# Kernel tuning notes

Measured on AMD Instinct MI355X. Metric: run time of the kernel, lower is better.

The kernel has to match this reference:

```python
import jax, jax.numpy as jnp
import numpy as np

N, V, E, C_IN, C_OUT = 4, 4096, 2048, 64, 64


def setup_inputs() -> dict:
    key = jax.random.key(0)
    k_x, k_h, k_th = jax.random.split(key, 3)
    x = jax.random.normal(k_x, (N, V, C_IN), dtype=jnp.float32)
    H = (jax.random.uniform(k_h, (N, V, E)) < 0.05).astype(jnp.float32)
    # guarantee every vertex and every hyperedge has degree >= 1 (code divides by degree)
    v_idx = jnp.arange(V)
    H = H.at[:, v_idx, v_idx % E].set(1.0)
    # xavier_uniform for theta
    limit = float(np.sqrt(6.0 / (C_IN + C_OUT)))
    theta = jax.random.uniform(k_th, (C_IN, C_OUT), minval=-limit, maxval=limit, dtype=jnp.float32)
    bias = jnp.zeros((C_OUT,), dtype=jnp.float32)
    return {"x": x, "H": H, "theta": theta, "bias": bias}


def reference(x, H, theta, bias):
    # x: [N,V,C], H: [N,V,E] incidence, theta: [C,O], bias: [O]
    # Original builds diag_embed(1/deg) and multiplies; equivalent to direct
    # per-row / per-column scaling of H (same math, no NxVxV / NxExE diagonals).
    dv = 1.0 / H.sum(-1)            # [N,V] vertex degrees
    de = 1.0 / H.sum(1)             # [N,E] hyperedge degrees
    y = jnp.einsum('nvc,co->nvo', x, theta)          # [N,V,O]
    HDe = H * de[:, None, :]                          # H @ De  -> [N,V,E]
    y = jnp.einsum('nvc,nve->nec', y, HDe)            # vertex -> edge  [N,E,O]
    HDv = H * dv[:, :, None]                          # Dv @ H -> [N,V,E]
    y = jnp.einsum('nec,nve->nvc', y, HDv)            # edge -> vertex  [N,V,O]
    return y + bias[None, None, :]
```

## Files before the change

kernel.cpp:

```cpp
#include <hip/hip_runtime.h>
#include <hip/hip_bf16.h>
#include <stdint.h>

#define N_B 4
#define NV 4096
#define NE 2048

typedef float    f32x4  __attribute__((ext_vector_type(4)));
typedef __bf16   bf16x8 __attribute__((ext_vector_type(8)));
typedef unsigned short u16;
typedef u16      u16x8  __attribute__((ext_vector_type(8)));
typedef uint32_t u32x4  __attribute__((ext_vector_type(4)));

__device__ __forceinline__ u16 f2bf_rne(float f) {
    uint32_t u = __builtin_bit_cast(uint32_t, f);
    u += 0x7FFFu + ((u >> 16) & 1u);
    return (u16)(u >> 16);
}
__device__ __forceinline__ float bf2f(u16 h) {
    uint32_t u = ((uint32_t)h) << 16;
    return __builtin_bit_cast(float, u);
}
__device__ __forceinline__ f32x4 mfma_bf16(u16x8 a, u16x8 b, f32x4 c) {
    return __builtin_amdgcn_mfma_f32_16x16x32_bf16(
        __builtin_bit_cast(bf16x8, a), __builtin_bit_cast(bf16x8, b), c, 0, 0, 0);
}
__device__ __forceinline__ u16x8 expand8(uint32_t byte) {
    u32x4 w;
#pragma unroll
    for (int p = 0; p < 4; ++p) {
        const uint32_t lo = (byte >> (2 * p)) & 1u;
        const uint32_t hi = (byte >> (2 * p + 1)) & 1u;
        w[p] = (lo | (hi << 16)) * 0x3F80u;
    }
    return __builtin_bit_cast(u16x8, w);
}

__global__ __launch_bounds__(256) void k_prep(const float* __restrict__ H,
                                              const float* __restrict__ x,
                                              const float* __restrict__ th,
                                              uint32_t* __restrict__ HB,
                                              uint32_t* __restrict__ HT,
                                              u16* __restrict__ Yh,
                                              u16* __restrict__ Yl) {
    __shared__ float smem[64 * 65];
    const int bid = blockIdx.x;
    const int t = threadIdx.x;

    if (bid < 8192) {
        float (*tile)[65] = (float(*)[65])smem;
        const int ex = bid & 31, vy = (bid >> 5) & 63, n = bid >> 11;
        const int e0 = ex * 64, v0 = vy * 64;
        const float* __restrict__ Hn = H + ((size_t)n * NV + v0) * NE + e0;

#pragma unroll
        for (int i = 0; i < 4; ++i) {
            const int idx = i * 256 + t;
            const int row = idx >> 4;
            const int q = (idx & 15) * 4;
            const float4 hv = *(const float4*)(Hn + (size_t)row * NE + q);
            tile[row][q] = hv.x; tile[row][q + 1] = hv.y;
            tile[row][q + 2] = hv.z; tile[row][q + 3] = hv.w;
        }
        __syncthreads();

        if (t < 128) {
            const int v = t >> 1, we = t & 1;
            uint32_t u = 0;
#pragma unroll
            for (int j = 0; j < 32; ++j)
                u |= (tile[v][we * 32 + j] != 0.0f) ? (1u << j) : 0u;
            HB[(((size_t)n * (NV / 16) + ((v0 + v) >> 4)) * (NE / 32) + (e0 >> 5) + we) * 16 +
               ((v0 + v) & 15)] = u;
        } else {
            const int e = (t - 128) >> 1, wv = t & 1;
            uint32_t u = 0;
#pragma unroll
            for (int j = 0; j < 32; ++j)
                u |= (tile[wv * 32 + j][e] != 0.0f) ? (1u << j) : 0u;
            HT[(((size_t)n * (NE / 16) + ((e0 + e) >> 4)) * (NV / 32) + (v0 >> 5) + wv) * 16 +
               ((e0 + e) & 15)] = u;
        }
    } else {
        float (*ts)[65] = (float(*)[65])smem;
        const int bx = bid - 8192;
        const int n = bx >> 6, v0 = (bx & 63) * 64;

#pragma unroll
        for (int i = 0; i < 4; ++i) {
            const int idx = i * 256 + t;
            const int row = idx >> 4, q = (idx & 15) * 4;
            const float4 tv = *(const float4*)&th[(size_t)row * 64 + q];
            ts[row][q] = tv.x; ts[row][q + 1] = tv.y;
            ts[row][q + 2] = tv.z; ts[row][q + 3] = tv.w;
        }
        __syncthreads();

        const int v4 = (t & 15) * 4;
        const int c4 = (t >> 4) * 4;
        const float* __restrict__ xb = x + ((size_t)(n * NV + v0 + v4)) * 64;

        float acc[4][4] = {};
#pragma unroll
        for (int kb = 0; kb < 16; ++kb) {
            float4 xr[4];
#pragma unroll
            for (int j = 0; j < 4; ++j)
                xr[j] = *(const float4*)(xb + (size_t)j * 64 + kb * 4);
#pragma unroll
            for (int kk = 0; kk < 4; ++kk) {
                const int k = kb * 4 + kk;
                float tv[4], xv[4];
#pragma unroll
                for (int i = 0; i < 4; ++i) tv[i] = ts[k][c4 + i];
                xv[0] = xr[0][kk]; xv[1] = xr[1][kk];
                xv[2] = xr[2][kk]; xv[3] = xr[3][kk];
#pragma unroll
                for (int i = 0; i < 4; ++i)
#pragma unroll
                    for (int j = 0; j < 4; ++j) acc[i][j] += tv[i] * xv[j];
            }
        }
#pragma unroll
        for (int i = 0; i < 4; ++i) {
            ushort4 hi, lo;
            u16 h;
            h = f2bf_rne(acc[i][0]); hi.x = h; lo.x = f2bf_rne(acc[i][0] - bf2f(h));
            h = f2bf_rne(acc[i][1]); hi.y = h; lo.y = f2bf_rne(acc[i][1] - bf2f(h));
            h = f2bf_rne(acc[i][2]); hi.z = h; lo.z = f2bf_rne(acc[i][2] - bf2f(h));
            h = f2bf_rne(acc[i][3]); hi.w = h; lo.w = f2bf_rne(acc[i][3] - bf2f(h));
            const size_t o = ((size_t)n * 64 + c4 + i) * NV + v0 + v4;
            *(ushort4*)&Yh[o] = hi;
            *(ushort4*)&Yl[o] = lo;
        }
    }
}

__global__ __launch_bounds__(256, 8) void k_v2e(const uint32_t* __restrict__ HT,
                                                const uint32_t* __restrict__ HB,
                                                const u16* __restrict__ Yh,
                                                const u16* __restrict__ Yl,
                                                float* __restrict__ P2,
                                                float* __restrict__ de,
                                                float* __restrict__ dv) {
    const int t = threadIdx.x;
    const int s2 = gridDim.y;
    const int lin = blockIdx.x + 32 * (blockIdx.y + s2 * blockIdx.z);
    const int nb = 32 * s2 * N_B;

    if (t < 64) {
        const int total = N_B * NE + N_B * NV;
        for (int id = lin * 64 + t; id < total; id += nb * 64) {
            if (id < N_B * NE) {
                const int n_ = id >> 11, e = id & (NE - 1);
                const uint32_t* p =
                    HT + ((size_t)n_ * (NE / 16) + (e >> 4)) * ((NV / 32) * 16) + (e & 15);
                uint32_t s = 0;
#pragma unroll 4
                for (int wv = 0; wv < NV / 32; ++wv) s += __popc(p[(size_t)wv * 16]);
                de[id] = (float)s;
            } else {
                const int j = id - N_B * NE;
                const int n_ = j >> 12, v = j & (NV - 1);
                const uint32_t* p =
                    HB + ((size_t)n_ * (NV / 16) + (v >> 4)) * ((NE / 32) * 16) + (v & 15);
                uint32_t s = 0;
#pragma unroll 4
                for (int we = 0; we < NE / 32; ++we) s += __popc(p[(size_t)we * 16]);
                dv[j] = (float)s;
            }
        }
    }

    const int wid = (lin & 7) * (nb >> 3) + (lin >> 3);
    const int n   = wid / (32 * s2);
    const int rem = wid % (32 * s2);
    const int sp  = rem >> 5;
    const int e0  = (rem & 31) * 64;

    const int krange = NV / s2;
    const int kk0 = sp * krange;
    const int S   = krange / 32;

    const int w = t >> 6, l = t & 63;
    const int lq = l >> 4, lr = l & 15;
    const int sh = lq * 8;
    const int hstride = (NV / 32) * 16;

    const uint32_t* __restrict__ ht =
        HT + ((size_t)n * (NE / 16) + (e0 >> 4)) * hstride + (kk0 >> 5) * 16 + lr;
    const u16* __restrict__ ybh = Yh + ((size_t)n * 64 + w * 16 + lr) * NV + kk0 + lq * 8;
    const u16* __restrict__ ybl = Yl + ((size_t)n * 64 + w * 16 + lr) * NV + kk0 + lq * 8;

    f32x4 acc0 = {0.f,0.f,0.f,0.f}, acc1 = acc0, acc2 = acc0, acc3 = acc0;

    uint32_t A[2][4];
#pragma unroll
    for (int d = 0; d < 2; ++d) {
        A[d][0] = ht[0 * hstride + d * 16];
        A[d][1] = ht[1 * hstride + d * 16];
        A[d][2] = ht[2 * hstride + d * 16];
        A[d][3] = ht[3 * hstride + d * 16];
    }
    u16x8 BH[2], BL[2];
    BH[0] = *(const u16x8*)ybh;
    BL[0] = *(const u16x8*)ybl;

#define V2E_STEP(s, u, GA, GB)                                                \
    {                                                                         \
        const uint32_t a0 = A[u][0], a1 = A[u][1], a2 = A[u][2], a3 = A[u][3];\
        if (GA) {                                                             \
            A[u][0] = ht[0 * hstride + ((s) + 2) * 16];                       \
            A[u][1] = ht[1 * hstride + ((s) + 2) * 16];                       \
            A[u][2] = ht[2 * hstride + ((s) + 2) * 16];                       \
            A[u][3] = ht[3 * hstride + ((s) + 2) * 16];                       \
        }                                                                     \
        if (GB) {                                                             \
            BH[((u) + 1) & 1] = *(const u16x8*)(ybh + ((s) + 1) * 32);        \
            BL[((u) + 1) & 1] = *(const u16x8*)(ybl + ((s) + 1) * 32);        \
        }                                                                     \
        const u16x8 bh = BH[u], bl = BL[u];                                   \
        u16x8 a;                                                              \
        a = expand8((a0 >> sh) & 0xFF);                                       \
        acc0 = mfma_bf16(a, bh, acc0); acc0 = mfma_bf16(a, bl, acc0);         \
        a = expand8((a1 >> sh) & 0xFF);                                       \
        acc1 = mfma_bf16(a, bh, acc1); acc1 = mfma_bf16(a, bl, acc1);         \
        a = expand8((a2 >> sh) & 0xFF);                                       \
        acc2 = mfma_bf16(a, bh, acc2); acc2 = mfma_bf16(a, bl, acc2);         \
        a = expand8((a3 >> sh) & 0xFF);                                       \
        acc3 = mfma_bf16(a, bh, acc3); acc3 = mfma_bf16(a, bl, acc3);         \
    }

    int sb = 0;
    for (; sb < S - 2; sb += 2) {
        V2E_STEP(sb + 0, 0, true, true)
        V2E_STEP(sb + 1, 1, true, true)
    }
    V2E_STEP(sb + 0, 0, false, true)
    V2E_STEP(sb + 1, 1, false, false)
#undef V2E_STEP

    float* pb = P2 + (((size_t)sp * N_B + n) * 64 + w * 16 + lr) * NE + e0 + lq * 4;
    *(f32x4*)(pb + 0)  = acc0;
    *(f32x4*)(pb + 16) = acc1;
    *(f32x4*)(pb + 32) = acc2;
    *(f32x4*)(pb + 48) = acc3;
}

__global__ __launch_bounds__(256) void k_red2(const float* __restrict__ P2,
                                              const float* __restrict__ de,
                                              u16* __restrict__ Zh,
                                              u16* __restrict__ Zl, int nsp) {
    const int i = blockIdx.x * 256 + threadIdx.x;
    const int row = i >> 9;
    const int e4  = (i & 511) * 4;
    const int n   = row >> 6;

    float4 a = make_float4(0.f, 0.f, 0.f, 0.f);
    for (int sp = 0; sp < nsp; ++sp) {
        const float4 p = *(const float4*)&P2[((size_t)sp * 256 + row) * NE + e4];
        a.x += p.x; a.y += p.y; a.z += p.z; a.w += p.w;
    }
    const float4 d = *(const float4*)&de[(size_t)n * NE + e4];
    float z[4] = {a.x / d.x, a.y / d.y, a.z / d.z, a.w / d.w};
    ushort4 hi, lo;
    u16 h;
    h = f2bf_rne(z[0]); hi.x = h; lo.x = f2bf_rne(z[0] - bf2f(h));
    h = f2bf_rne(z[1]); hi.y = h; lo.y = f2bf_rne(z[1] - bf2f(h));
    h = f2bf_rne(z[2]); hi.z = h; lo.z = f2bf_rne(z[2] - bf2f(h));
    h = f2bf_rne(z[3]); hi.w = h; lo.w = f2bf_rne(z[3] - bf2f(h));
    *(ushort4*)&Zh[(size_t)row * NE + e4] = hi;
    *(ushort4*)&Zl[(size_t)row * NE + e4] = lo;
}

__global__ __launch_bounds__(256, 8) void k_e2v(const uint32_t* __restrict__ HB,
                                                const u16* __restrict__ Zh,
                                                const u16* __restrict__ Zl,
                                                float* __restrict__ P3) {
    const int t = threadIdx.x;
    const int s3 = gridDim.y;
    const int lin = blockIdx.x + 64 * (blockIdx.y + s3 * blockIdx.z);
    const int nb = 64 * s3 * N_B;

    const int wid = (lin & 7) * (nb >> 3) + (lin >> 3);
    const int n   = wid / (64 * s3);
    const int rem = wid % (64 * s3);
    const int sp  = rem >> 6;
    const int v0  = (rem & 63) * 64;

    const int krange = NE / s3;
    const int kk0 = sp * krange;
    const int S   = krange / 32;

    const int w = t >> 6, l = t & 63;
    const int lq = l >> 4, lr = l & 15;
    const int sh = lq * 8;
    const int estride = (NE / 32) * 16;

    const uint32_t* __restrict__ hb =
        HB + ((size_t)n * (NV / 16) + (v0 >> 4)) * estride + (kk0 >> 5) * 16 + lr;
    const u16* __restrict__ zbh = Zh + ((size_t)n * 64 + w * 16 + lr) * NE + kk0 + lq * 8;
    const u16* __restrict__ zbl = Zl + ((size_t)n * 64 + w * 16 + lr) * NE + kk0 + lq * 8;

    f32x4 acc0 = {0.f,0.f,0.f,0.f}, acc1 = acc0, acc2 = acc0, acc3 = acc0;

    uint32_t A[2][4];
#pragma unroll
    for (int d = 0; d < 2; ++d) {
        A[d][0] = hb[0 * estride + d * 16];
        A[d][1] = hb[1 * estride + d * 16];
        A[d][2] = hb[2 * estride + d * 16];
        A[d][3] = hb[3 * estride + d * 16];
    }
    u16x8 BH[2], BL[2];
    BH[0] = *(const u16x8*)zbh;
    BL[0] = *(const u16x8*)zbl;

#define E2V_STEP(s, u, GA, GB)                                                \
    {                                                                         \
        const uint32_t a0 = A[u][0], a1 = A[u][1], a2 = A[u][2], a3 = A[u][3];\
        if (GA) {                                                             \
            A[u][0] = hb[0 * estride + ((s) + 2) * 16];                       \
            A[u][1] = hb[1 * estride + ((s) + 2) * 16];                       \
            A[u][2] = hb[2 * estride + ((s) + 2) * 16];                       \
            A[u][3] = hb[3 * estride + ((s) + 2) * 16];                       \
        }                                                                     \
        if (GB) {                                                             \
            BH[((u) + 1) & 1] = *(const u16x8*)(zbh + ((s) + 1) * 32);        \
            BL[((u) + 1) & 1] = *(const u16x8*)(zbl + ((s) + 1) * 32);        \
        }                                                                     \
        const u16x8 bh = BH[u], bl = BL[u];                                   \
        u16x8 a;                                                              \
        a = expand8((a0 >> sh) & 0xFF);                                       \
        acc0 = mfma_bf16(a, bh, acc0); acc0 = mfma_bf16(a, bl, acc0);         \
        a = expand8((a1 >> sh) & 0xFF);                                       \
        acc1 = mfma_bf16(a, bh, acc1); acc1 = mfma_bf16(a, bl, acc1);         \
        a = expand8((a2 >> sh) & 0xFF);                                       \
        acc2 = mfma_bf16(a, bh, acc2); acc2 = mfma_bf16(a, bl, acc2);         \
        a = expand8((a3 >> sh) & 0xFF);                                       \
        acc3 = mfma_bf16(a, bh, acc3); acc3 = mfma_bf16(a, bl, acc3);         \
    }

    int sb = 0;
    for (; sb < S - 2; sb += 2) {
        E2V_STEP(sb + 0, 0, true, true)
        E2V_STEP(sb + 1, 1, true, true)
    }
    E2V_STEP(sb + 0, 0, false, true)
    E2V_STEP(sb + 1, 1, false, false)
#undef E2V_STEP

    float* pb = P3 + (((size_t)sp * N_B + n) * 64 + w * 16 + lr) * NV + v0 + lq * 4;
    *(f32x4*)(pb + 0)  = acc0;
    *(f32x4*)(pb + 16) = acc1;
    *(f32x4*)(pb + 32) = acc2;
    *(f32x4*)(pb + 48) = acc3;
}

__global__ __launch_bounds__(512) void k_red3(const float* __restrict__ P3,
                                              const float* __restrict__ dv,
                                              const float* __restrict__ bias,
                                              float* __restrict__ out, int nsp) {
    __shared__ float lt[64][68];
    const int n  = blockIdx.y;
    const int v0 = blockIdx.x * 64;
    const int t  = threadIdx.x;

    {
        const int c   = t >> 3;
        const int vch = (t & 7) * 8;
        float4 s0 = make_float4(0.f, 0.f, 0.f, 0.f), s1 = s0;
        for (int sp = 0; sp < nsp; ++sp) {
            const size_t base = (((size_t)sp * N_B + n) * 64 + c) * NV + v0 + vch;
            const float4 p0 = *(const float4*)&P3[base];
            const float4 p1 = *(const float4*)&P3[base + 4];
            s0.x += p0.x; s0.y += p0.y; s0.z += p0.z; s0.w += p0.w;
            s1.x += p1.x; s1.y += p1.y; s1.z += p1.z; s1.w += p1.w;
        }
        *(float4*)&lt[c][vch]     = s0;
        *(float4*)&lt[c][vch + 4] = s1;
    }
    const int vw  = t >> 3;
    const int cch = (t & 7) * 8;
    const float dsum = dv[(size_t)n * NV + v0 + vw];
    __syncthreads();

    const float rdv = 1.0f / dsum;
    const float4 b0 = *(const float4*)&bias[cch];
    const float4 b1 = *(const float4*)&bias[cch + 4];
    float4 o0, o1;
    o0.x = lt[cch + 0][vw] * rdv + b0.x;
    o0.y = lt[cch + 1][vw] * rdv + b0.y;
    o0.z = lt[cch + 2][vw] * rdv + b0.z;
    o0.w = lt[cch + 3][vw] * rdv + b0.w;
    o1.x = lt[cch + 4][vw] * rdv + b1.x;
    o1.y = lt[cch + 5][vw] * rdv + b1.y;
    o1.z = lt[cch + 6][vw] * rdv + b1.z;
    o1.w = lt[cch + 7][vw] * rdv + b1.w;
    float* dst = out + ((size_t)n * NV + v0 + vw) * 64 + cch;
    *(float4*)dst       = o0;
    *(float4*)(dst + 4) = o1;
}

extern "C" void kernel_launch(void* const* d_in, const int* in_sizes, int n_in,
                              void* d_out, int out_size, void* d_ws, size_t ws_size,
                              hipStream_t stream) {
    const float* x     = (const float*)d_in[0];
    const float* H     = (const float*)d_in[1];
    const float* theta = (const float*)d_in[2];
    const float* bias  = (const float*)d_in[3];
    float* out = (float*)d_out;

    const size_t yE  = (size_t)N_B * 64 * NV;
    const size_t zE  = (size_t)N_B * 64 * NE;
    const size_t HBW = (size_t)N_B * (NV / 16) * (NE / 32) * 16;
    const size_t HTW = (size_t)N_B * (NE / 16) * (NV / 32) * 16;
    const size_t deE = (size_t)N_B * NE;
    const size_t dvE = (size_t)N_B * NV;

    u16* Yh = (u16*)d_ws;
    u16* Yl = Yh + yE;
    u16* Zh = Yl + yE;
    u16* Zl = Zh + zE;
    uint32_t* HB = (uint32_t*)(Zl + zE);
    uint32_t* HT = HB + HBW;
    float* de = (float*)(HT + HTW);
    float* dv = de + deE;
    float* fbase = dv + dvE;

    const size_t fixed_bytes = (size_t)((char*)fbase - (char*)d_ws);
    const size_t avail_f = (ws_size > fixed_bytes) ? (ws_size - fixed_bytes) / 4 : 0;

    int s2 = 2, s3 = 1;
    if      (avail_f >= 16 * zE + 8 * yE) { s2 = 16; s3 = 8; }
    else if (avail_f >=  8 * zE + 4 * yE) { s2 = 8;  s3 = 4; }
    else if (avail_f >=  4 * zE + 2 * yE) { s2 = 4;  s3 = 2; }

    float* P2 = fbase;
    float* P3 = P2 + (size_t)s2 * zE;

    k_prep<<<dim3(8192 + 256), 256, 0, stream>>>(H, x, theta, HB, HT, Yh, Yl);
    k_v2e<<<dim3(NE / 64, s2, N_B), 256, 0, stream>>>(HT, HB, Yh, Yl, P2, de, dv);
    k_red2<<<dim3((int)(zE / 4 / 256)), 256, 0, stream>>>(P2, de, Zh, Zl, s2);
    k_e2v<<<dim3(NV / 64, s3, N_B), 256, 0, stream>>>(HB, Zh, Zl, P3);
    k_red3<<<dim3(NV / 64, N_B), 512, 0, stream>>>(P3, dv, bias, out, s3);
}
```

Before: 112.3 us.

## Process four H tiles per prep block with register-prefetched software pipelining

The H-to-bitmask prep stage now has each block handle four 64x64 tiles instead of one, cutting the grid from 8192 to 2048 blocks. The next tile's global loads go into registers while the current tile's bitmasks are built from shared memory, so load latency overlaps with compute. Row-mask building now reads float4 vectors from LDS. The costs are more barriers per block, higher register pressure, and fewer blocks to hide latency across the GPU. Since this stage streams 128MB of H, it is likely memory-bound, which limits what can be gained.

```diff
diff --git a/kernel.cpp b/kernel.cpp
--- a/kernel.cpp
+++ b/kernel.cpp
@@ -47,43 +47,86 @@
     const int bid = blockIdx.x;
     const int t = threadIdx.x;
 
-    if (bid < 8192) {
+    if (bid < 2048) {
         float (*tile)[65] = (float(*)[65])smem;
-        const int ex = bid & 31, vy = (bid >> 5) & 63, n = bid >> 11;
-        const int e0 = ex * 64, v0 = vy * 64;
-        const float* __restrict__ Hn = H + ((size_t)n * NV + v0) * NE + e0;
-
-#pragma unroll
-        for (int i = 0; i < 4; ++i) {
-            const int idx = i * 256 + t;
-            const int row = idx >> 4;
-            const int q = (idx & 15) * 4;
-            const float4 hv = *(const float4*)(Hn + (size_t)row * NE + q);
-            tile[row][q] = hv.x; tile[row][q + 1] = hv.y;
-            tile[row][q + 2] = hv.z; tile[row][q + 3] = hv.w;
-        }
-        __syncthreads();
-
-        if (t < 128) {
-            const int v = t >> 1, we = t & 1;
-            uint32_t u = 0;
-#pragma unroll
-            for (int j = 0; j < 32; ++j)
-                u |= (tile[v][we * 32 + j] != 0.0f) ? (1u << j) : 0u;
-            HB[(((size_t)n * (NV / 16) + ((v0 + v) >> 4)) * (NE / 32) + (e0 >> 5) + we) * 16 +
-               ((v0 + v) & 15)] = u;
-        } else {
-            const int e = (t - 128) >> 1, wv = t & 1;
-            uint32_t u = 0;
-#pragma unroll
-            for (int j = 0; j < 32; ++j)
-                u |= (tile[wv * 32 + j][e] != 0.0f) ? (1u << j) : 0u;
-            HT[(((size_t)n * (NE / 16) + ((e0 + e) >> 4)) * (NV / 32) + (v0 >> 5) + wv) * 16 +
-               ((e0 + e) & 15)] = u;
-        }
+        const int srow = t >> 4;
+        const int sq   = (t & 15) * 4;
+        float4 R0, R1, R2, R3;
+
+#define LOADT(tid)                                                            \
+        {                                                                     \
+            const int ex_ = (tid) & 31, vy_ = ((tid) >> 5) & 63, n_ = (tid) >> 11; \
+            const float* __restrict__ Hn_ =                                   \
+                H + ((size_t)n_ * NV + vy_ * 64) * NE + ex_ * 64;             \
+            R0 = *(const float4*)(Hn_ + (size_t)(srow +  0) * NE + sq);       \
+            R1 = *(const float4*)(Hn_ + (size_t)(srow + 16) * NE + sq);       \
+            R2 = *(const float4*)(Hn_ + (size_t)(srow + 32) * NE + sq);       \
+            R3 = *(const float4*)(Hn_ + (size_t)(srow + 48) * NE + sq);       \
+        }
+#define STORET()                                                              \
+        {                                                                     \
+            *(float4*)&tile[srow +  0][sq] = R0;                              \
+            *(float4*)&tile[srow + 16][sq] = R1;                              \
+            *(float4*)&tile[srow + 32][sq] = R2;                              \
+            *(float4*)&tile[srow + 48][sq] = R3;                              \
+        }
+#define BUILDT(tid)                                                           \
+        {                                                                     \
+            const int ex_ = (tid) & 31, vy_ = ((tid) >> 5) & 63, n_ = (tid) >> 11; \
+            const int e0_ = ex_ * 64, v0_ = vy_ * 64;                         \
+            if (t < 128) {                                                    \
+                const int v = t >> 1, we = t & 1;                             \
+                uint32_t u = 0;                                               \
+                _Pragma("unroll")                                             \
+                for (int q = 0; q < 8; ++q) {                                 \
+                    const f32x4 f = *(const f32x4*)&tile[v][we * 32 + q * 4]; \
+                    u |= (f[0] != 0.0f ? 1u : 0u) << (4 * q + 0);             \
+                    u |= (f[1] != 0.0f ? 1u : 0u) << (4 * q + 1);             \
+                    u |= (f[2] != 0.0f ? 1u : 0u) << (4 * q + 2);             \
+                    u |= (f[3] != 0.0f ? 1u : 0u) << (4 * q + 3);             \
+                }                                                             \
+                HB[(((size_t)n_ * (NV / 16) + ((v0_ + v) >> 4)) * (NE / 32) + \
+                    (e0_ >> 5) + we) * 16 + ((v0_ + v) & 15)] = u;            \
+            } else {                                                          \
+                const int e = (t - 128) >> 1, wv = t & 1;                     \
+                uint32_t u = 0;                                               \
+                _Pragma("unroll")                                             \
+                for (int j = 0; j < 32; ++j)                                  \
+                    u |= (tile[wv * 32 + j][e] != 0.0f) ? (1u << j) : 0u;     \
+                HT[(((size_t)n_ * (NE / 16) + ((e0_ + e) >> 4)) * (NV / 32) + \
+                    (v0_ >> 5) + wv) * 16 + ((e0_ + e) & 15)] = u;            \
+            }                                                                 \
+        }
+
+        LOADT(bid * 4 + 0)
+        __syncthreads();
+        STORET()
+        __syncthreads();
+        LOADT(bid * 4 + 1)
+        BUILDT(bid * 4 + 0)
+
+        __syncthreads();
+        STORET()
+        __syncthreads();
+        LOADT(bid * 4 + 2)
+        BUILDT(bid * 4 + 1)
+
+        __syncthreads();
+        STORET()
+        __syncthreads();
+        LOADT(bid * 4 + 3)
+        BUILDT(bid * 4 + 2)
+
+        __syncthreads();
+        STORET()
+        __syncthreads();
+        BUILDT(bid * 4 + 3)
+#undef LOADT
+#undef STORET
+#undef BUILDT
     } else {
         float (*ts)[65] = (float(*)[65])smem;
-        const int bx = bid - 8192;
+        const int bx = bid - 2048;
         const int n = bx >> 6, v0 = (bx & 63) * 64;
 
 #pragma unroll
@@ -439,7 +482,7 @@
     float* P2 = fbase;
     float* P3 = P2 + (size_t)s2 * zE;
 
-    k_prep<<<dim3(8192 + 256), 256, 0, stream>>>(H, x, theta, HB, HT, Yh, Yl);
+    k_prep<<<dim3(2048 + 256), 256, 0, stream>>>(H, x, theta, HB, HT, Yh, Yl);
     k_v2e<<<dim3(NE / 64, s2, N_B), 256, 0, stream>>>(HT, HB, Yh, Yl, P2, de, dv);
     k_red2<<<dim3((int)(zE / 4 / 256)), 256, 0, stream>>>(P2, de, Zh, Zl, s2);
     k_e2v<<<dim3(NV / 64, s3, N_B), 256, 0, stream>>>(HB, Zh, Zl, P3);
```

Result: faster. 107.3 us (-4.4%).
